# Performance work log

Hardware: AMD Instinct MI355X
Metric: run time of the kernel (lower is better)

## Reference

```python
import jax, jax.numpy as jnp
import numpy as np

DIM = 1024
N_HEADS = 16
HEAD_DIM = DIM // N_HEADS


def setup_inputs() -> dict:
    key = jax.random.key(0)
    ks = jax.random.split(key, 5)
    x = jax.random.normal(ks[0], (2, 2048, DIM), dtype=jnp.float32)
    # nn.Linear-style init scale
    s = 1.0 / np.sqrt(DIM)
    W_qkv = jax.random.uniform(ks[1], (DIM, 3 * DIM), jnp.float32, -s, s)
    b_qkv = jax.random.uniform(ks[2], (3 * DIM,), jnp.float32, -s, s)
    W_proj = jax.random.uniform(ks[3], (DIM, DIM), jnp.float32, -s, s)
    b_proj = jax.random.uniform(ks[4], (DIM,), jnp.float32, -s, s)
    return {"x": x, "W_qkv": W_qkv, "b_qkv": b_qkv, "W_proj": W_proj, "b_proj": b_proj}


def reference(x, W_qkv, b_qkv, W_proj, b_proj):
    B, S, D = x.shape
    scale = HEAD_DIM ** -0.5
    qkv = x @ W_qkv + b_qkv                                   # [B,S,3D]
    qkv = qkv.reshape(B, S, 3, N_HEADS, HEAD_DIM)
    q = qkv[:, :, 0].transpose(0, 2, 1, 3)                    # [B,H,S,d]
    k = qkv[:, :, 1].transpose(0, 2, 1, 3)
    v = qkv[:, :, 2].transpose(0, 2, 1, 3)
    attn = jnp.einsum('bhqd,bhkd->bhqk', q, k) * scale        # [B,H,S,S]
    attn = jax.nn.softmax(attn, axis=-1)
    out = jnp.einsum('bhqk,bhkd->bhqd', attn, v)              # [B,H,S,d]
    out = out.transpose(0, 2, 1, 3).reshape(B, S, D)
    return out @ W_proj + b_proj
```

## Files before the change

kernel.cpp:

```cpp
#include <hip/hip_runtime.h>
#include <stdint.h>

typedef unsigned short u16;
typedef __attribute__((ext_vector_type(8))) short bf16x8;
typedef __attribute__((ext_vector_type(4))) float f32x4;
typedef __attribute__((ext_vector_type(16))) float f32x16;
typedef __attribute__((ext_vector_type(4))) u16 us4;
typedef __attribute__((ext_vector_type(8))) u16 us8;

__device__ __forceinline__ u16 f2bf(float f) {
  union { float f; unsigned u; } v; v.f = f;
  unsigned r = v.u + 0x7fffu + ((v.u >> 16) & 1u);
  return (u16)(r >> 16);
}

__device__ __forceinline__ float bf2f(u16 b) {
  union { float f; unsigned u; } v; v.u = ((unsigned)b) << 16;
  return v.f;
}

__device__ __forceinline__ unsigned pkbf(float a, float b) {
  union { float f; unsigned u; } x, y; x.f = a; y.f = b;
  return __builtin_amdgcn_perm(y.u + 0x8000u, x.u + 0x8000u, 0x07060302u);
}

__device__ __forceinline__ float fast_exp2(float x) {
#if __has_builtin(__builtin_amdgcn_exp2f)
  return __builtin_amdgcn_exp2f(x);
#else
  return exp2f(x);
#endif
}

__device__ __forceinline__ void gld16(const void* g, void* l) {
  __builtin_amdgcn_global_load_lds(
      (const __attribute__((address_space(1))) void*)g,
      (__attribute__((address_space(3))) void*)l, 16, 0, 0);
}

__global__ void prep_kernel(const float* __restrict__ x, u16* __restrict__ Xb,
                            const float* __restrict__ Wqkv, u16* __restrict__ Wqkt,
                            const float* __restrict__ Wproj, u16* __restrict__ Wpt) {
  __shared__ u16 tile[32][33];
  const int blk = blockIdx.x;
  if (blk < 4096) {
    const int i = blk * 256 + threadIdx.x;
    f32x4 v = ((const f32x4*)x)[i];
    us4 r;
#pragma unroll
    for (int j = 0; j < 4; ++j) r[j] = f2bf(v[j]);
    ((us4*)Xb)[i] = r;
    return;
  }
  const float* in;
  u16* out;
  int R, C, t;
  if (blk < 7168) { in = Wqkv; out = Wqkt; R = 1024; C = 3072; t = blk - 4096; }
  else            { in = Wproj; out = Wpt; R = 1024; C = 1024; t = blk - 7168; }
  const int gx = (C == 3072) ? (t % 96) : (t % 32);
  const int gy = (C == 3072) ? (t / 96) : (t / 32);
  const int tx = threadIdx.x & 31, ty = threadIdx.x >> 5;
  const int c0 = gx * 32, r0 = gy * 32;
#pragma unroll
  for (int j = 0; j < 4; ++j)
    tile[ty + j * 8][tx] = f2bf(in[(size_t)(r0 + ty + j * 8) * C + c0 + tx]);
  __syncthreads();
#pragma unroll
  for (int j = 0; j < 4; ++j)
    out[(size_t)(c0 + ty + j * 8) * R + r0 + tx] = tile[tx][ty + j * 8];
}

__global__ __launch_bounds__(256) void qkv_gemm_kernel(
    const u16* __restrict__ A, const u16* __restrict__ Bt, const float* __restrict__ bias,
    u16* __restrict__ Qb, u16* __restrict__ Kb, u16* __restrict__ Vtb) {
  __shared__ u16 sm[17408];
  u16* As = sm;
  u16* Bs = sm + 4096;
  const int tid = threadIdx.x;
  const int w = tid >> 6, l = tid & 63, quad = l >> 4, lanelo = l & 15;
  const int wr = w >> 1, wc = w & 1;
  const int flat = blockIdx.x + 32 * blockIdx.y;
  const int xcd = flat & 7, lid = flat >> 3;
  const long m0 = (long)((xcd >> 1) * 8 + (lid & 7)) * 128;
  const long n0 = (long)((xcd & 1) * 12 + (lid >> 3)) * 128;

  f32x4 acc[4][4];
#pragma unroll
  for (int i = 0; i < 4; ++i)
#pragma unroll
    for (int j = 0; j < 4; ++j) acc[i][j] = (f32x4){0.f, 0.f, 0.f, 0.f};

  const u16* ag = A + (m0 + w * 32 + (l >> 2)) * 1024 + (l & 3) * 8;
  const u16* bg = Bt + (n0 + w * 32 + (l >> 2)) * 1024 + (l & 3) * 8;
  u16* asl = As + w * 1024;
  u16* bsl = Bs + w * 1024;

  for (int kt = 0; kt < 32; ++kt) {
    const int ko = kt * 32;
    gld16(ag + ko, asl);
    gld16(ag + 16 * 1024 + ko, asl + 512);
    gld16(bg + ko, bsl);
    gld16(bg + 16 * 1024 + ko, bsl + 512);
    __syncthreads();
    bf16x8 af[4], bf[4];
#pragma unroll
    for (int mt = 0; mt < 4; ++mt)
      af[mt] = *(const bf16x8*)(As + (wr * 64 + mt * 16 + lanelo) * 32 + quad * 8);
#pragma unroll
    for (int nt = 0; nt < 4; ++nt)
      bf[nt] = *(const bf16x8*)(Bs + (wc * 64 + nt * 16 + lanelo) * 32 + quad * 8);
#pragma unroll
    for (int mt = 0; mt < 4; ++mt)
#pragma unroll
      for (int nt = 0; nt < 4; ++nt)
        acc[mt][nt] = __builtin_amdgcn_mfma_f32_16x16x32_bf16(af[mt], bf[nt], acc[mt][nt], 0, 0, 0);
    __syncthreads();
  }

  const int t = (int)(n0 >> 10);
  const float scl = (t == 0) ? 0.18033688011112042f : 1.0f;

  float bias_v[4];
#pragma unroll
  for (int nt = 0; nt < 4; ++nt) bias_v[nt] = bias[n0 + wc * 64 + nt * 16 + lanelo];

  u16* Ct = sm;
#pragma unroll
  for (int mt = 0; mt < 4; ++mt)
#pragma unroll
    for (int nt = 0; nt < 4; ++nt)
#pragma unroll
      for (int r = 0; r < 4; ++r)
        Ct[(wr * 64 + mt * 16 + quad * 4 + r) * 136 + wc * 64 + nt * 16 + lanelo] =
            f2bf((acc[mt][nt][r] + bias_v[nt]) * scl);
  __syncthreads();

  const int b = (int)(m0 >> 11);
  const int s0 = (int)(m0 & 2047);
  const int h0 = (int)((n0 & 1023) >> 6);

  if (t < 2) {
    u16* dst = (t == 0) ? Qb : Kb;
#pragma unroll
    for (int p = 0; p < 8; ++p) {
      const int hh = p >> 2;
      const int sl = (p & 3) * 32 + (tid >> 3);
      const int c8 = tid & 7;
      us8 v = *(const us8*)(Ct + sl * 136 + hh * 64 + c8 * 8);
      const int pos = (c8 + sl) & 7;
      const size_t off = ((size_t)((b * 16 + h0 + hh) * 2048 + s0 + sl)) * 64 + pos * 8;
      *(us8*)(dst + off) = v;
    }
  } else {
#pragma unroll
    for (int p = 0; p < 8; ++p) {
      const int hh = p >> 2;
      const int dl = (p & 3) * 16 + (tid >> 4);
      const int c16 = tid & 15;
      us8 v;
#pragma unroll
      for (int j = 0; j < 8; ++j) v[j] = Ct[(c16 * 8 + j) * 136 + hh * 64 + dl];
      const int pos = (c16 + dl) & 15;
      const size_t off = ((size_t)((b * 16 + h0 + hh) * 64 + dl)) * 2048 + s0 + pos * 8;
      *(us8*)(Vtb + off) = v;
    }
  }
}

__global__ __launch_bounds__(256, 4) void attn_kernel(
    const u16* __restrict__ Qb, const u16* __restrict__ Kb,
    const u16* __restrict__ Vtb, u16* __restrict__ Op, float* __restrict__ lp) {
  __shared__ u16 Ks[8192];
  __shared__ u16 Vs[8192];
  const int tid = threadIdx.x;
  const int w = tid >> 6, l = tid & 63;
  const int m = l & 31, hi = l >> 5;
  const int fid = blockIdx.x;
  const int head = (fid & 7) + 8 * ((fid >> 3) & 3);
  const int qt = (fid >> 5) & 15;
  const int z = fid >> 9;
  const u16* Qh = Qb + (size_t)head * 2048 * 64;
  const u16* Kh = Kb + (size_t)head * 2048 * 64;
  const u16* Vh = Vtb + (size_t)head * 64 * 2048;
  const int permaddr = (l ^ 32) << 2;

  const int qrow = qt * 128 + w * 32 + m;
  bf16x8 qf[4];
#pragma unroll
  for (int ks = 0; ks < 4; ++ks) {
    const int c = ks * 2 + hi;
    const int pos = (c + qrow) & 7;
    qf[ks] = *(const bf16x8*)(Qh + (size_t)qrow * 64 + pos * 8);
  }

  f32x16 o0, o1;
#pragma unroll
  for (int i = 0; i < 16; ++i) { o0[i] = 0.f; o1[i] = 0.f; }
  float sacc = 0.f;

  for (int kt = 0; kt < 8; ++kt) {
    const int kb = z * 8 + kt;
    const u16* kbase = Kh + (size_t)kb * 8192;
#pragma unroll
    for (int j = 0; j < 4; ++j) {
      const int i = w * 4 + j;
      gld16(kbase + i * 512 + l * 8, &Ks[i * 512]);
    }
#pragma unroll
    for (int j = 0; j < 4; ++j) {
      const int i = w * 4 + j;
      const int dd = i * 4 + (l >> 4);
      gld16(Vh + (size_t)dd * 2048 + kb * 128 + (l & 15) * 8, &Vs[i * 512]);
    }
    __syncthreads();

#pragma unroll
    for (int g = 0; g < 4; ++g) {
      f32x16 st;
#pragma unroll
      for (int i = 0; i < 16; ++i) st[i] = 0.f;
      const int key = g * 32 + m;
#pragma unroll
      for (int ks = 0; ks < 4; ++ks) {
        const int c = ks * 2 + hi;
        const int pos = (c + key) & 7;
        bf16x8 kf = *(const bf16x8*)(&Ks[key * 64 + pos * 8]);
        st = __builtin_amdgcn_mfma_f32_32x32x16_bf16(kf, qf[ks], st, 0, 0, 0);
      }

      float p[16];
#pragma unroll
      for (int r = 0; r < 16; ++r) p[r] = fast_exp2(st[r]);
#pragma unroll
      for (int r = 0; r < 16; ++r) sacc += p[r];

      unsigned L[8];
#pragma unroll
      for (int q4 = 0; q4 < 4; ++q4) {
        L[2 * q4] = pkbf(p[4 * q4], p[4 * q4 + 1]);
        L[2 * q4 + 1] = pkbf(p[4 * q4 + 2], p[4 * q4 + 3]);
      }

#pragma unroll
      for (int s = 0; s < 2; ++s) {
        const unsigned a0 = L[4 * s], a1 = L[4 * s + 1];
        const unsigned b0 = L[4 * s + 2], b1 = L[4 * s + 3];
        const unsigned s0 = hi ? a0 : b0;
        const unsigned s1 = hi ? a1 : b1;
        const unsigned r0 = (unsigned)__builtin_amdgcn_ds_bpermute(permaddr, (int)s0);
        const unsigned r1 = (unsigned)__builtin_amdgcn_ds_bpermute(permaddr, (int)s1);
        int4 fd;
        fd.x = (int)(hi ? r0 : a0);
        fd.y = (int)(hi ? r1 : a1);
        fd.z = (int)(hi ? b0 : r0);
        fd.w = (int)(hi ? b1 : r1);
        union { int4 i; bf16x8 v; } pu; pu.i = fd;
        const int c = g * 4 + s * 2 + hi;
#pragma unroll
        for (int n = 0; n < 2; ++n) {
          const int d = n * 32 + m;
          const int pos = (c + d) & 15;
          bf16x8 vf = *(const bf16x8*)(&Vs[d * 128 + pos * 8]);
          if (n == 0) o0 = __builtin_amdgcn_mfma_f32_32x32x16_bf16(pu.v, vf, o0, 0, 0, 0);
          else        o1 = __builtin_amdgcn_mfma_f32_32x32x16_bf16(pu.v, vf, o1, 0, 0, 0);
        }
      }
    }
    __syncthreads();
  }

  union { float f; int i; } sv; sv.f = sacc;
  union { float f; int i; } pv; pv.i = __builtin_amdgcn_ds_bpermute(permaddr, sv.i);
  const float ltot = sacc + pv.f;
  if (hi == 0)
    lp[(size_t)z * 65536 + (size_t)head * 2048 + qt * 128 + w * 32 + m] = ltot;

  const int b = head >> 4, h = head & 15;
  u16* Od = Op + (size_t)z * 4194304;
#pragma unroll
  for (int r = 0; r < 16; ++r) {
    const int qlocal = (r & 3) + 8 * (r >> 2) + 4 * hi;
    const size_t base =
        ((size_t)(b * 2048 + qt * 128 + w * 32 + qlocal)) * 1024 + h * 64;
    Od[base + m] = f2bf(o0[r]);
    Od[base + 32 + m] = f2bf(o1[r]);
  }
}

__global__ __launch_bounds__(128) void combine_kernel(
    const u16* __restrict__ Op, const float* __restrict__ lp, u16* __restrict__ Ob) {
  const int r = blockIdx.x;
  const int tid = threadIdx.x;
  const int col = tid * 8;
  const int b = r >> 11, s = r & 2047, h = col >> 6;
  const size_t li = (size_t)(b * 16 + h) * 2048 + s;
  const float linv = 1.0f / (lp[li] + lp[65536 + li]);
  us8 v0 = *(const us8*)(Op + (size_t)r * 1024 + col);
  us8 v1 = *(const us8*)(Op + 4194304 + (size_t)r * 1024 + col);
  us8 o;
#pragma unroll
  for (int j = 0; j < 8; ++j)
    o[j] = f2bf((bf2f(v0[j]) + bf2f(v1[j])) * linv);
  *(us8*)(Ob + (size_t)r * 1024 + col) = o;
}

__global__ __launch_bounds__(256) void proj_gemm_kernel(
    const u16* __restrict__ A, const u16* __restrict__ Bt,
    const float* __restrict__ bias, float* __restrict__ out) {
  __shared__ u16 sm[6144];
  u16* As = sm;
  u16* Bs = sm + 4096;
  const int tid = threadIdx.x;
  const int w = tid >> 6, l = tid & 63, quad = l >> 4, lanelo = l & 15;
  const int wr = w >> 1, wc = w & 1;
  const int flat = blockIdx.x + 32 * blockIdx.y;
  const int xcd = flat & 7, lid = flat >> 3;
  const long m0 = (long)(xcd * 4 + (lid & 3)) * 128;
  const long n0 = (long)(lid >> 2) * 64;

  f32x4 acc[4][2];
#pragma unroll
  for (int i = 0; i < 4; ++i)
#pragma unroll
    for (int j = 0; j < 2; ++j) acc[i][j] = (f32x4){0.f, 0.f, 0.f, 0.f};

  const u16* ag = A + (m0 + w * 32 + (l >> 2)) * 1024 + (l & 3) * 8;
  const u16* bg = Bt + (n0 + w * 16 + (l >> 2)) * 1024 + (l & 3) * 8;
  u16* asl = As + w * 1024;
  u16* bsl = Bs + w * 512;

  for (int kt = 0; kt < 32; ++kt) {
    const int ko = kt * 32;
    gld16(ag + ko, asl);
    gld16(ag + 16 * 1024 + ko, asl + 512);
    gld16(bg + ko, bsl);
    __syncthreads();
    bf16x8 af[4], bf[2];
#pragma unroll
    for (int mt = 0; mt < 4; ++mt)
      af[mt] = *(const bf16x8*)(As + (wr * 64 + mt * 16 + lanelo) * 32 + quad * 8);
#pragma unroll
    for (int nt = 0; nt < 2; ++nt)
      bf[nt] = *(const bf16x8*)(Bs + (wc * 32 + nt * 16 + lanelo) * 32 + quad * 8);
#pragma unroll
    for (int mt = 0; mt < 4; ++mt)
#pragma unroll
      for (int nt = 0; nt < 2; ++nt)
        acc[mt][nt] = __builtin_amdgcn_mfma_f32_16x16x32_bf16(af[mt], bf[nt], acc[mt][nt], 0, 0, 0);
    __syncthreads();
  }

  float bias_v[2];
#pragma unroll
  for (int nt = 0; nt < 2; ++nt)
    bias_v[nt] = bias[n0 + wc * 32 + nt * 16 + lanelo];

#pragma unroll
  for (int mt = 0; mt < 4; ++mt)
#pragma unroll
    for (int nt = 0; nt < 2; ++nt)
#pragma unroll
      for (int r = 0; r < 4; ++r) {
        const size_t mm = m0 + wr * 64 + mt * 16 + quad * 4 + r;
        const size_t nn = n0 + wc * 32 + nt * 16 + lanelo;
        out[mm * 1024 + nn] = acc[mt][nt][r] + bias_v[nt];
      }
}

extern "C" void kernel_launch(void* const* d_in, const int* in_sizes, int n_in,
                              void* d_out, int out_size, void* d_ws, size_t ws_size,
                              hipStream_t stream) {
  const float* x = (const float*)d_in[0];
  const float* Wqkv = (const float*)d_in[1];
  const float* bqkv = (const float*)d_in[2];
  const float* Wproj = (const float*)d_in[3];
  const float* bproj = (const float*)d_in[4];
  float* out = (float*)d_out;
  char* ws = (char*)d_ws;

  u16* Xb   = (u16*)(ws);
  u16* Op   = (u16*)(ws);
  u16* Wqkt = (u16*)(ws + 8388608);
  u16* Qb   = (u16*)(ws + 16777216);
  u16* Ob   = (u16*)(ws + 16777216);
  u16* Kb   = (u16*)(ws + 25165824);
  u16* Vtb  = (u16*)(ws + 33554432);
  u16* Wpt  = (u16*)(ws + 41943040);
  float* lp = (float*)(ws + 44040192);

  prep_kernel<<<8192, 256, 0, stream>>>(x, Xb, Wqkv, Wqkt, Wproj, Wpt);
  qkv_gemm_kernel<<<dim3(32, 24), 256, 0, stream>>>(Xb, Wqkt, bqkv, Qb, Kb, Vtb);
  attn_kernel<<<1024, 256, 0, stream>>>(Qb, Kb, Vtb, Op, lp);
  combine_kernel<<<4096, 128, 0, stream>>>(Op, lp, Ob);
  proj_gemm_kernel<<<dim3(32, 16), 256, 0, stream>>>(Ob, Wpt, bproj, out);
}
```

Measured before the change: 188.4 us.

## Double-buffer attention K/V tiles, drop P bpermute, fuse combine into projection GEMM

The attention kernel now double-buffers its K and V shared-memory tiles and prefetches the next tile after a single barrier per iteration, overlapping loads with MFMA work. The P-operand lane exchange via ds_bpermute is replaced by reading V with split 4-element loads arranged to match the P register layout. The separate combine kernel is removed: the projection GEMM reads both split-K partial outputs, normalizes them by the summed softmax denominators, and writes the result into its A tile. This saves a launch and an intermediate round trip, but the GEMM's A loads become synchronous register loads, and double buffering doubles LDS use, which may lower occupancy.

```diff
diff --git a/kernel.cpp b/kernel.cpp
--- a/kernel.cpp
+++ b/kernel.cpp
@@ -170,8 +170,8 @@
 __global__ __launch_bounds__(256, 4) void attn_kernel(
     const u16* __restrict__ Qb, const u16* __restrict__ Kb,
     const u16* __restrict__ Vtb, u16* __restrict__ Op, float* __restrict__ lp) {
-  __shared__ u16 Ks[8192];
-  __shared__ u16 Vs[8192];
+  __shared__ u16 Ks[2][8192];
+  __shared__ u16 Vs[2][8192];
   const int tid = threadIdx.x;
   const int w = tid >> 6, l = tid & 63;
   const int m = l & 31, hi = l >> 5;
@@ -188,8 +188,7 @@
   bf16x8 qf[4];
 #pragma unroll
   for (int ks = 0; ks < 4; ++ks) {
-    const int c = ks * 2 + hi;
-    const int pos = (c + qrow) & 7;
+    const int pos = (ks * 2 + hi + qrow) & 7;
     qf[ks] = *(const bf16x8*)(Qh + (size_t)qrow * 64 + pos * 8);
   }
 
@@ -198,21 +197,42 @@
   for (int i = 0; i < 16; ++i) { o0[i] = 0.f; o1[i] = 0.f; }
   float sacc = 0.f;
 
-  for (int kt = 0; kt < 8; ++kt) {
-    const int kb = z * 8 + kt;
+  {
+    const int kb = z * 8;
     const u16* kbase = Kh + (size_t)kb * 8192;
 #pragma unroll
     for (int j = 0; j < 4; ++j) {
       const int i = w * 4 + j;
-      gld16(kbase + i * 512 + l * 8, &Ks[i * 512]);
+      gld16(kbase + i * 512 + l * 8, &Ks[0][i * 512]);
     }
 #pragma unroll
     for (int j = 0; j < 4; ++j) {
       const int i = w * 4 + j;
       const int dd = i * 4 + (l >> 4);
-      gld16(Vh + (size_t)dd * 2048 + kb * 128 + (l & 15) * 8, &Vs[i * 512]);
-    }
+      gld16(Vh + (size_t)dd * 2048 + kb * 128 + (l & 15) * 8, &Vs[0][i * 512]);
+    }
+  }
+
+  for (int kt = 0; kt < 8; ++kt) {
     __syncthreads();
+    if (kt < 7) {
+      const int kb = z * 8 + kt + 1;
+      const int tb = (kt + 1) & 1;
+      const u16* kbase = Kh + (size_t)kb * 8192;
+#pragma unroll
+      for (int j = 0; j < 4; ++j) {
+        const int i = w * 4 + j;
+        gld16(kbase + i * 512 + l * 8, &Ks[tb][i * 512]);
+      }
+#pragma unroll
+      for (int j = 0; j < 4; ++j) {
+        const int i = w * 4 + j;
+        const int dd = i * 4 + (l >> 4);
+        gld16(Vh + (size_t)dd * 2048 + kb * 128 + (l & 15) * 8, &Vs[tb][i * 512]);
+      }
+    }
+    const u16* Kc = &Ks[kt & 1][0];
+    const u16* Vc = &Vs[kt & 1][0];
 
 #pragma unroll
     for (int g = 0; g < 4; ++g) {
@@ -222,9 +242,8 @@
       const int key = g * 32 + m;
 #pragma unroll
       for (int ks = 0; ks < 4; ++ks) {
-        const int c = ks * 2 + hi;
-        const int pos = (c + key) & 7;
-        bf16x8 kf = *(const bf16x8*)(&Ks[key * 64 + pos * 8]);
+        const int pos = (ks * 2 + hi + key) & 7;
+        bf16x8 kf = *(const bf16x8*)(&Kc[key * 64 + pos * 8]);
         st = __builtin_amdgcn_mfma_f32_32x32x16_bf16(kf, qf[ks], st, 0, 0, 0);
       }
 
@@ -242,31 +261,24 @@
       }
 
 #pragma unroll
-      for (int s = 0; s < 2; ++s) {
-        const unsigned a0 = L[4 * s], a1 = L[4 * s + 1];
-        const unsigned b0 = L[4 * s + 2], b1 = L[4 * s + 3];
-        const unsigned s0 = hi ? a0 : b0;
-        const unsigned s1 = hi ? a1 : b1;
-        const unsigned r0 = (unsigned)__builtin_amdgcn_ds_bpermute(permaddr, (int)s0);
-        const unsigned r1 = (unsigned)__builtin_amdgcn_ds_bpermute(permaddr, (int)s1);
-        int4 fd;
-        fd.x = (int)(hi ? r0 : a0);
-        fd.y = (int)(hi ? r1 : a1);
-        fd.z = (int)(hi ? b0 : r0);
-        fd.w = (int)(hi ? b1 : r1);
-        union { int4 i; bf16x8 v; } pu; pu.i = fd;
-        const int c = g * 4 + s * 2 + hi;
+      for (int t = 0; t < 2; ++t) {
+        union { unsigned u[4]; bf16x8 v; } af;
+#pragma unroll
+        for (int j = 0; j < 4; ++j) af.u[j] = L[4 * t + j];
+        const int c0 = g * 4 + t * 2;
 #pragma unroll
         for (int n = 0; n < 2; ++n) {
           const int d = n * 32 + m;
-          const int pos = (c + d) & 15;
-          bf16x8 vf = *(const bf16x8*)(&Vs[d * 128 + pos * 8]);
-          if (n == 0) o0 = __builtin_amdgcn_mfma_f32_32x32x16_bf16(pu.v, vf, o0, 0, 0, 0);
-          else        o1 = __builtin_amdgcn_mfma_f32_32x32x16_bf16(pu.v, vf, o1, 0, 0, 0);
+          const int pos0 = (c0 + d) & 15;
+          const int pos1 = (c0 + 1 + d) & 15;
+          union { us4 q[2]; bf16x8 v; } vf;
+          vf.q[0] = *(const us4*)(&Vc[d * 128 + pos0 * 8 + hi * 4]);
+          vf.q[1] = *(const us4*)(&Vc[d * 128 + pos1 * 8 + hi * 4]);
+          if (n == 0) o0 = __builtin_amdgcn_mfma_f32_32x32x16_bf16(af.v, vf.v, o0, 0, 0, 0);
+          else        o1 = __builtin_amdgcn_mfma_f32_32x32x16_bf16(af.v, vf.v, o1, 0, 0, 0);
         }
       }
     }
-    __syncthreads();
   }
 
   union { float f; int i; } sv; sv.f = sacc;
@@ -287,26 +299,10 @@
   }
 }
 
-__global__ __launch_bounds__(128) void combine_kernel(
-    const u16* __restrict__ Op, const float* __restrict__ lp, u16* __restrict__ Ob) {
-  const int r = blockIdx.x;
-  const int tid = threadIdx.x;
-  const int col = tid * 8;
-  const int b = r >> 11, s = r & 2047, h = col >> 6;
-  const size_t li = (size_t)(b * 16 + h) * 2048 + s;
-  const float linv = 1.0f / (lp[li] + lp[65536 + li]);
-  us8 v0 = *(const us8*)(Op + (size_t)r * 1024 + col);
-  us8 v1 = *(const us8*)(Op + 4194304 + (size_t)r * 1024 + col);
-  us8 o;
-#pragma unroll
-  for (int j = 0; j < 8; ++j)
-    o[j] = f2bf((bf2f(v0[j]) + bf2f(v1[j])) * linv);
-  *(us8*)(Ob + (size_t)r * 1024 + col) = o;
-}
-
 __global__ __launch_bounds__(256) void proj_gemm_kernel(
-    const u16* __restrict__ A, const u16* __restrict__ Bt,
-    const float* __restrict__ bias, float* __restrict__ out) {
+    const u16* __restrict__ Op, const float* __restrict__ lp,
+    const u16* __restrict__ Bt, const float* __restrict__ bias,
+    float* __restrict__ out) {
   __shared__ u16 sm[6144];
   u16* As = sm;
   u16* Bs = sm + 4096;
@@ -324,30 +320,53 @@
 #pragma unroll
     for (int j = 0; j < 2; ++j) acc[i][j] = (f32x4){0.f, 0.f, 0.f, 0.f};
 
-  const u16* ag = A + (m0 + w * 32 + (l >> 2)) * 1024 + (l & 3) * 8;
+  const int r0 = (int)m0 + w * 32 + (l >> 2);
+  const int r1 = r0 + 16;
+  const int c8 = (l & 3) * 8;
+  const int bb = r0 >> 11;
+  const int s0r = r0 & 2047, s1r = r1 & 2047;
+  const u16* A0 = Op;
+  const u16* A1 = Op + 4194304;
+
   const u16* bg = Bt + (n0 + w * 16 + (l >> 2)) * 1024 + (l & 3) * 8;
-  u16* asl = As + w * 1024;
   u16* bsl = Bs + w * 512;
-
-  for (int kt = 0; kt < 32; ++kt) {
-    const int ko = kt * 32;
-    gld16(ag + ko, asl);
-    gld16(ag + 16 * 1024 + ko, asl + 512);
-    gld16(bg + ko, bsl);
-    __syncthreads();
-    bf16x8 af[4], bf[2];
-#pragma unroll
-    for (int mt = 0; mt < 4; ++mt)
-      af[mt] = *(const bf16x8*)(As + (wr * 64 + mt * 16 + lanelo) * 32 + quad * 8);
-#pragma unroll
-    for (int nt = 0; nt < 2; ++nt)
-      bf[nt] = *(const bf16x8*)(Bs + (wc * 32 + nt * 16 + lanelo) * 32 + quad * 8);
-#pragma unroll
-    for (int mt = 0; mt < 4; ++mt)
+  u16* awr = As + w * 1024 + l * 8;
+
+  for (int h = 0; h < 16; ++h) {
+    const size_t lbase = (size_t)(bb * 16 + h) * 2048;
+    const float li0 = 1.0f / (lp[lbase + s0r] + lp[65536 + lbase + s0r]);
+    const float li1 = 1.0f / (lp[lbase + s1r] + lp[65536 + lbase + s1r]);
+#pragma unroll
+    for (int sub = 0; sub < 2; ++sub) {
+      const int ko = (h * 2 + sub) * 32;
+      us8 x0 = *(const us8*)(A0 + (size_t)r0 * 1024 + ko + c8);
+      us8 y0 = *(const us8*)(A1 + (size_t)r0 * 1024 + ko + c8);
+      us8 x1 = *(const us8*)(A0 + (size_t)r1 * 1024 + ko + c8);
+      us8 y1 = *(const us8*)(A1 + (size_t)r1 * 1024 + ko + c8);
+      gld16(bg + ko, bsl);
+      us8 o0s, o1s;
+#pragma unroll
+      for (int j = 0; j < 8; ++j) {
+        o0s[j] = f2bf((bf2f(x0[j]) + bf2f(y0[j])) * li0);
+        o1s[j] = f2bf((bf2f(x1[j]) + bf2f(y1[j])) * li1);
+      }
+      *(us8*)(awr) = o0s;
+      *(us8*)(awr + 512) = o1s;
+      __syncthreads();
+      bf16x8 af[4], bf[2];
+#pragma unroll
+      for (int mt = 0; mt < 4; ++mt)
+        af[mt] = *(const bf16x8*)(As + (wr * 64 + mt * 16 + lanelo) * 32 + quad * 8);
 #pragma unroll
       for (int nt = 0; nt < 2; ++nt)
-        acc[mt][nt] = __builtin_amdgcn_mfma_f32_16x16x32_bf16(af[mt], bf[nt], acc[mt][nt], 0, 0, 0);
-    __syncthreads();
+        bf[nt] = *(const bf16x8*)(Bs + (wc * 32 + nt * 16 + lanelo) * 32 + quad * 8);
+#pragma unroll
+      for (int mt = 0; mt < 4; ++mt)
+#pragma unroll
+        for (int nt = 0; nt < 2; ++nt)
+          acc[mt][nt] = __builtin_amdgcn_mfma_f32_16x16x32_bf16(af[mt], bf[nt], acc[mt][nt], 0, 0, 0);
+      __syncthreads();
+    }
   }
 
   float bias_v[2];
@@ -382,7 +401,6 @@
   u16* Op   = (u16*)(ws);
   u16* Wqkt = (u16*)(ws + 8388608);
   u16* Qb   = (u16*)(ws + 16777216);
-  u16* Ob   = (u16*)(ws + 16777216);
   u16* Kb   = (u16*)(ws + 25165824);
   u16* Vtb  = (u16*)(ws + 33554432);
   u16* Wpt  = (u16*)(ws + 41943040);
@@ -391,6 +409,5 @@
   prep_kernel<<<8192, 256, 0, stream>>>(x, Xb, Wqkv, Wqkt, Wproj, Wpt);
   qkv_gemm_kernel<<<dim3(32, 24), 256, 0, stream>>>(Xb, Wqkt, bqkv, Qb, Kb, Vtb);
   attn_kernel<<<1024, 256, 0, stream>>>(Qb, Kb, Vtb, Op, lp);
-  combine_kernel<<<4096, 128, 0, stream>>>(Op, lp, Ob);
-  proj_gemm_kernel<<<dim3(32, 16), 256, 0, stream>>>(Ob, Wpt, bproj, out);
-}
+  proj_gemm_kernel<<<dim3(32, 16), 256, 0, stream>>>(Op, lp, Wpt, bproj, out);
+}
```

Measured after the change: 204.6 us. 8.6% more time.

## Double-buffer K/V tiles in LDS to overlap global loads with MFMA

Applied to the files above, without the earlier changes.

The attention kernel now splits each 128-key tile into two 64-key halves held in two ping-pong LDS buffers, using the same total LDS. It issues the async global-to-LDS load for the next half before computing the current one, and needs only one barrier per iteration. The goal is to hide K/V load latency behind the QK and PV MFMA work. The trade-off is twice as many iterations and barriers, plus remapped V addressing and swizzles that must match the layout written by the producer kernel.

```diff
diff --git a/kernel.cpp b/kernel.cpp
--- a/kernel.cpp
+++ b/kernel.cpp
@@ -170,8 +170,8 @@
 __global__ __launch_bounds__(256, 4) void attn_kernel(
     const u16* __restrict__ Qb, const u16* __restrict__ Kb,
     const u16* __restrict__ Vtb, u16* __restrict__ Op, float* __restrict__ lp) {
-  __shared__ u16 Ks[8192];
-  __shared__ u16 Vs[8192];
+  __shared__ u16 Ks[2][4096];
+  __shared__ u16 Vs[2][4096];
   const int tid = threadIdx.x;
   const int w = tid >> 6, l = tid & 63;
   const int m = l & 31, hi = l >> 5;
@@ -188,43 +188,69 @@
   bf16x8 qf[4];
 #pragma unroll
   for (int ks = 0; ks < 4; ++ks) {
-    const int c = ks * 2 + hi;
-    const int pos = (c + qrow) & 7;
+    const int pos = (ks * 2 + hi + qrow) & 7;
     qf[ks] = *(const bf16x8*)(Qh + (size_t)qrow * 64 + pos * 8);
   }
+
+  const int kslot = w * 2;
+  const int d0 = w * 16 + (l >> 3);
+  const int pos8l = l & 7;
+  const int c8st = (pos8l - d0) & 7;
 
   f32x16 o0, o1;
 #pragma unroll
   for (int i = 0; i < 16; ++i) { o0[i] = 0.f; o1[i] = 0.f; }
   float sacc = 0.f;
 
-  for (int kt = 0; kt < 8; ++kt) {
-    const int kb = z * 8 + kt;
-    const u16* kbase = Kh + (size_t)kb * 8192;
-#pragma unroll
-    for (int j = 0; j < 4; ++j) {
-      const int i = w * 4 + j;
-      gld16(kbase + i * 512 + l * 8, &Ks[i * 512]);
+  {
+    const int kb = z * 1024;
+    const int kb128 = z * 8;
+#pragma unroll
+    for (int j = 0; j < 2; ++j)
+      gld16(Kh + (size_t)kb * 64 + (kslot + j) * 512 + l * 8,
+            &Ks[0][(kslot + j) * 512 + l * 8]);
+#pragma unroll
+    for (int j = 0; j < 2; ++j) {
+      const int d = d0 + j * 8;
+      const int pos16 = (c8st + d) & 15;
+      gld16(Vh + (size_t)d * 2048 + kb128 * 128 + pos16 * 8,
+            &Vs[0][(kslot + j) * 512 + l * 8]);
     }
-#pragma unroll
-    for (int j = 0; j < 4; ++j) {
-      const int i = w * 4 + j;
-      const int dd = i * 4 + (l >> 4);
-      gld16(Vh + (size_t)dd * 2048 + kb * 128 + (l & 15) * 8, &Vs[i * 512]);
+  }
+
+  for (int t = 0; t < 16; ++t) {
+    __syncthreads();
+    if (t < 15) {
+      const int tn = t + 1;
+      const int tb = tn & 1;
+      const int kb = z * 1024 + tn * 64;
+      const int kb128 = z * 8 + (tn >> 1);
+      const int hsel = (tn & 1) * 8;
+#pragma unroll
+      for (int j = 0; j < 2; ++j)
+        gld16(Kh + (size_t)kb * 64 + (kslot + j) * 512 + l * 8,
+              &Ks[tb][(kslot + j) * 512 + l * 8]);
+#pragma unroll
+      for (int j = 0; j < 2; ++j) {
+        const int d = d0 + j * 8;
+        const int pos16 = (hsel + c8st + d) & 15;
+        gld16(Vh + (size_t)d * 2048 + kb128 * 128 + pos16 * 8,
+              &Vs[tb][(kslot + j) * 512 + l * 8]);
+      }
     }
-    __syncthreads();
-
-#pragma unroll
-    for (int g = 0; g < 4; ++g) {
+    const u16* Kc = &Ks[t & 1][0];
+    const u16* Vc = &Vs[t & 1][0];
+
+#pragma unroll
+    for (int g = 0; g < 2; ++g) {
       f32x16 st;
 #pragma unroll
       for (int i = 0; i < 16; ++i) st[i] = 0.f;
       const int key = g * 32 + m;
 #pragma unroll
       for (int ks = 0; ks < 4; ++ks) {
-        const int c = ks * 2 + hi;
-        const int pos = (c + key) & 7;
-        bf16x8 kf = *(const bf16x8*)(&Ks[key * 64 + pos * 8]);
+        const int pos = (ks * 2 + hi + key) & 7;
+        bf16x8 kf = *(const bf16x8*)(&Kc[key * 64 + pos * 8]);
         st = __builtin_amdgcn_mfma_f32_32x32x16_bf16(kf, qf[ks], st, 0, 0, 0);
       }
 
@@ -259,14 +285,13 @@
 #pragma unroll
         for (int n = 0; n < 2; ++n) {
           const int d = n * 32 + m;
-          const int pos = (c + d) & 15;
-          bf16x8 vf = *(const bf16x8*)(&Vs[d * 128 + pos * 8]);
+          const int pos = (c + d) & 7;
+          bf16x8 vf = *(const bf16x8*)(&Vc[d * 64 + pos * 8]);
           if (n == 0) o0 = __builtin_amdgcn_mfma_f32_32x32x16_bf16(pu.v, vf, o0, 0, 0, 0);
           else        o1 = __builtin_amdgcn_mfma_f32_32x32x16_bf16(pu.v, vf, o1, 0, 0, 0);
         }
       }
     }
-    __syncthreads();
   }
 
   union { float f; int i; } sv; sv.f = sacc;
```

New measurement: 192.1 us. No clear change (+2.0%).

## Fuse split-K attention halves into one block and drop combine kernel

Applied to the files above, without the earlier changes.

Both key-range halves of the attention for a query tile now run as two 4-wave groups inside one 512-thread block. The second group's partial output and row sums pass through shared memory, and the first group normalizes and writes the final bf16 output. This removes the combine kernel launch and the global round trip of two bf16 partial outputs plus the row-sum buffer. In exchange it doubles LDS per block and halves the block count. The final reduction also adds a block barrier and a serialized epilogue.

```diff
diff --git a/kernel.cpp b/kernel.cpp
--- a/kernel.cpp
+++ b/kernel.cpp
@@ -167,18 +167,19 @@
   }
 }
 
-__global__ __launch_bounds__(256, 4) void attn_kernel(
+__global__ __launch_bounds__(512, 4) void attn_kernel(
     const u16* __restrict__ Qb, const u16* __restrict__ Kb,
-    const u16* __restrict__ Vtb, u16* __restrict__ Op, float* __restrict__ lp) {
-  __shared__ u16 Ks[8192];
-  __shared__ u16 Vs[8192];
+    const u16* __restrict__ Vtb, u16* __restrict__ Ob) {
+  __shared__ u16 Ks[2][8192];
+  __shared__ u16 Vs[2][8192];
   const int tid = threadIdx.x;
-  const int w = tid >> 6, l = tid & 63;
+  const int w8 = tid >> 6;
+  const int z = w8 >> 2, w = w8 & 3;
+  const int l = tid & 63;
   const int m = l & 31, hi = l >> 5;
   const int fid = blockIdx.x;
   const int head = (fid & 7) + 8 * ((fid >> 3) & 3);
-  const int qt = (fid >> 5) & 15;
-  const int z = fid >> 9;
+  const int qt = fid >> 5;
   const u16* Qh = Qb + (size_t)head * 2048 * 64;
   const u16* Kh = Kb + (size_t)head * 2048 * 64;
   const u16* Vh = Vtb + (size_t)head * 64 * 2048;
@@ -188,8 +189,7 @@
   bf16x8 qf[4];
 #pragma unroll
   for (int ks = 0; ks < 4; ++ks) {
-    const int c = ks * 2 + hi;
-    const int pos = (c + qrow) & 7;
+    const int pos = (ks * 2 + hi + qrow) & 7;
     qf[ks] = *(const bf16x8*)(Qh + (size_t)qrow * 64 + pos * 8);
   }
 
@@ -204,13 +204,13 @@
 #pragma unroll
     for (int j = 0; j < 4; ++j) {
       const int i = w * 4 + j;
-      gld16(kbase + i * 512 + l * 8, &Ks[i * 512]);
+      gld16(kbase + i * 512 + l * 8, &Ks[z][i * 512]);
     }
 #pragma unroll
     for (int j = 0; j < 4; ++j) {
       const int i = w * 4 + j;
       const int dd = i * 4 + (l >> 4);
-      gld16(Vh + (size_t)dd * 2048 + kb * 128 + (l & 15) * 8, &Vs[i * 512]);
+      gld16(Vh + (size_t)dd * 2048 + kb * 128 + (l & 15) * 8, &Vs[z][i * 512]);
     }
     __syncthreads();
 
@@ -222,9 +222,8 @@
       const int key = g * 32 + m;
 #pragma unroll
       for (int ks = 0; ks < 4; ++ks) {
-        const int c = ks * 2 + hi;
-        const int pos = (c + key) & 7;
-        bf16x8 kf = *(const bf16x8*)(&Ks[key * 64 + pos * 8]);
+        const int pos = (ks * 2 + hi + key) & 7;
+        bf16x8 kf = *(const bf16x8*)(&Ks[z][key * 64 + pos * 8]);
         st = __builtin_amdgcn_mfma_f32_32x32x16_bf16(kf, qf[ks], st, 0, 0, 0);
       }
 
@@ -260,7 +259,7 @@
         for (int n = 0; n < 2; ++n) {
           const int d = n * 32 + m;
           const int pos = (c + d) & 15;
-          bf16x8 vf = *(const bf16x8*)(&Vs[d * 128 + pos * 8]);
+          bf16x8 vf = *(const bf16x8*)(&Vs[z][d * 128 + pos * 8]);
           if (n == 0) o0 = __builtin_amdgcn_mfma_f32_32x32x16_bf16(pu.v, vf, o0, 0, 0, 0);
           else        o1 = __builtin_amdgcn_mfma_f32_32x32x16_bf16(pu.v, vf, o1, 0, 0, 0);
         }
@@ -272,36 +271,37 @@
   union { float f; int i; } sv; sv.f = sacc;
   union { float f; int i; } pv; pv.i = __builtin_amdgcn_ds_bpermute(permaddr, sv.i);
   const float ltot = sacc + pv.f;
-  if (hi == 0)
-    lp[(size_t)z * 65536 + (size_t)head * 2048 + qt * 128 + w * 32 + m] = ltot;
-
-  const int b = head >> 4, h = head & 15;
-  u16* Od = Op + (size_t)z * 4194304;
-#pragma unroll
-  for (int r = 0; r < 16; ++r) {
-    const int qlocal = (r & 3) + 8 * (r >> 2) + 4 * hi;
-    const size_t base =
-        ((size_t)(b * 2048 + qt * 128 + w * 32 + qlocal)) * 1024 + h * 64;
-    Od[base + m] = f2bf(o0[r]);
-    Od[base + 32 + m] = f2bf(o1[r]);
-  }
-}
-
-__global__ __launch_bounds__(128) void combine_kernel(
-    const u16* __restrict__ Op, const float* __restrict__ lp, u16* __restrict__ Ob) {
-  const int r = blockIdx.x;
-  const int tid = threadIdx.x;
-  const int col = tid * 8;
-  const int b = r >> 11, s = r & 2047, h = col >> 6;
-  const size_t li = (size_t)(b * 16 + h) * 2048 + s;
-  const float linv = 1.0f / (lp[li] + lp[65536 + li]);
-  us8 v0 = *(const us8*)(Op + (size_t)r * 1024 + col);
-  us8 v1 = *(const us8*)(Op + 4194304 + (size_t)r * 1024 + col);
-  us8 o;
-#pragma unroll
-  for (int j = 0; j < 8; ++j)
-    o[j] = f2bf((bf2f(v0[j]) + bf2f(v1[j])) * linv);
-  *(us8*)(Ob + (size_t)r * 1024 + col) = o;
+
+  float* Osl = (float*)Ks;
+  float* Lz1 = (float*)Vs;
+
+  if (z == 1) {
+    if (hi == 0) Lz1[w * 32 + m] = ltot;
+#pragma unroll
+    for (int r = 0; r < 16; ++r) {
+      const int qlocal = (r & 3) + 8 * (r >> 2) + 4 * hi;
+      Osl[w * 2048 + qlocal * 64 + m] = o0[r];
+      Osl[w * 2048 + qlocal * 64 + 32 + m] = o1[r];
+    }
+  }
+  __syncthreads();
+  if (z == 0) {
+    const float lfull = ltot + Lz1[w * 32 + m];
+    union { float f; int i; } li; li.f = 1.0f / lfull;
+    const int b = head >> 4, h = head & 15;
+#pragma unroll
+    for (int r = 0; r < 16; ++r) {
+      const int qlocal = (r & 3) + 8 * (r >> 2) + 4 * hi;
+      union { float f; int i; } lg;
+      lg.i = __builtin_amdgcn_ds_bpermute(qlocal << 2, li.i);
+      const float v0 = (o0[r] + Osl[w * 2048 + qlocal * 64 + m]) * lg.f;
+      const float v1 = (o1[r] + Osl[w * 2048 + qlocal * 64 + 32 + m]) * lg.f;
+      const size_t base =
+          ((size_t)(b * 2048 + qt * 128 + w * 32 + qlocal)) * 1024 + h * 64;
+      Ob[base + m] = f2bf(v0);
+      Ob[base + 32 + m] = f2bf(v1);
+    }
+  }
 }
 
 __global__ __launch_bounds__(256) void proj_gemm_kernel(
@@ -379,18 +379,15 @@
   char* ws = (char*)d_ws;
 
   u16* Xb   = (u16*)(ws);
-  u16* Op   = (u16*)(ws);
+  u16* Ob   = (u16*)(ws);
   u16* Wqkt = (u16*)(ws + 8388608);
   u16* Qb   = (u16*)(ws + 16777216);
-  u16* Ob   = (u16*)(ws + 16777216);
   u16* Kb   = (u16*)(ws + 25165824);
   u16* Vtb  = (u16*)(ws + 33554432);
   u16* Wpt  = (u16*)(ws + 41943040);
-  float* lp = (float*)(ws + 44040192);
 
   prep_kernel<<<8192, 256, 0, stream>>>(x, Xb, Wqkv, Wqkt, Wproj, Wpt);
   qkv_gemm_kernel<<<dim3(32, 24), 256, 0, stream>>>(Xb, Wqkt, bqkv, Qb, Kb, Vtb);
-  attn_kernel<<<1024, 256, 0, stream>>>(Qb, Kb, Vtb, Op, lp);
-  combine_kernel<<<4096, 128, 0, stream>>>(Op, lp, Ob);
+  attn_kernel<<<512, 512, 0, stream>>>(Qb, Kb, Vtb, Ob);
   proj_gemm_kernel<<<dim3(32, 16), 256, 0, stream>>>(Ob, Wpt, bproj, out);
 }
```

Result: no change. 187.0 us (-0.7%).
